# Optimization experiments

Measured on AMD Instinct MI355X. Metric: run time of the kernel, lower is better.

The kernel has to match this reference:

```python
import jax, jax.numpy as jnp
import numpy as np

NODES = 23   # 22 players + ball per frame-graph
K = 8        # random neighbors per node
B, T = 64, 128
G = B * T            # total graphs (frames)
N = G * NODES        # total nodes
D_IN, H, RH = 16, 128, 128


def setup_inputs() -> dict:
    key = jax.random.key(0)
    ks = jax.random.split(key, 10)
    x = jax.random.normal(ks[0], (N, D_IN), jnp.float32)
    # per-graph random edges: dst = each node repeated K times, src = random node in same graph
    src_local = jax.random.randint(ks[1], (G, NODES * K), 0, NODES)
    dst_local = jnp.tile(jnp.repeat(jnp.arange(NODES), K)[None, :], (G, 1))
    off = (jnp.arange(G) * NODES)[:, None]
    edge_index = jnp.stack([(src_local + off).reshape(-1),
                            (dst_local + off).reshape(-1)]).astype(jnp.int32)
    runner_idx = jax.random.randint(ks[2], (G,), 0, NODES, dtype=jnp.int32)
    sc = lambda k, sh: (jax.random.normal(k, sh, jnp.float32) * 0.05)
    return {
        'x': x, 'edge_index': edge_index, 'runner_idx': runner_idx,
        'W1': sc(ks[3], (D_IN, H)), 'b1': jnp.zeros((H,), jnp.float32),
        'W2': sc(ks[4], (H, H)),    'b2': jnp.zeros((H,), jnp.float32),
        'W_ih': sc(ks[5], (3 * RH, H)), 'W_hh': sc(ks[6], (3 * RH, RH)),
        'b_ih': jnp.zeros((3 * RH,), jnp.float32), 'b_hh': jnp.zeros((3 * RH,), jnp.float32),
        'Wp': sc(ks[7], (RH, 2)), 'bp': jnp.zeros((2,), jnp.float32),
    }


def _gcn_conv(h, edge_index, W, b):
    # PyG GCNConv: add self-loops, symmetric normalization, scatter-sum
    h = h @ W
    loop = jnp.arange(N, dtype=edge_index.dtype)
    s = jnp.concatenate([edge_index[0], loop])
    d = jnp.concatenate([edge_index[1], loop])
    deg = jax.ops.segment_sum(jnp.ones_like(s, h.dtype), d, num_segments=N)
    dinv = jnp.where(deg > 0, jax.lax.rsqrt(deg), 0.0)
    norm = dinv[s] * dinv[d]                      # [E+N]
    out = jax.ops.segment_sum(h[s] * norm[:, None], d, num_segments=N)
    return out + b


def _gru(seq, W_ih, W_hh, b_ih, b_hh):
    # torch GRU: gates in r,z,n order
    xg = seq @ W_ih.T + b_ih                      # [B,T,3RH]
    def step(hprev, xt):
        gh = hprev @ W_hh.T + b_hh
        xr, xz, xn = jnp.split(xt, 3, axis=-1)
        hr, hz, hn = jnp.split(gh, 3, axis=-1)
        r = jax.nn.sigmoid(xr + hr)
        z = jax.nn.sigmoid(xz + hz)
        n = jnp.tanh(xn + r * hn)
        hnew = (1.0 - z) * n + z * hprev
        return hnew, hnew
    h0 = jnp.zeros((seq.shape[0], RH), seq.dtype)
    _, outs = jax.lax.scan(step, h0, jnp.swapaxes(xg, 0, 1))
    return jnp.swapaxes(outs, 0, 1)               # [B,T,RH]


def reference(x, edge_index, runner_idx, W1, b1, W2, b2,
              W_ih, W_hh, b_ih, b_hh, Wp, bp):
    h = jax.nn.relu(_gcn_conv(x, edge_index, W1, b1))
    h = jax.nn.relu(_gcn_conv(h, edge_index, W2, b2))
    # fused equivalent of the per-graph nonzero()/indexing loop:
    runner_global = jnp.arange(G, dtype=jnp.int32) * NODES + runner_idx
    seq = h[runner_global].reshape(B, T, H)       # all lengths == T, padding is a no-op
    out = _gru(seq, W_ih, W_hh, b_ih, b_hh)
    return out @ Wp + bp                          # [B,T,2]
```

## Files before the change

### kernel.cpp

```cpp
#include <hip/hip_runtime.h>
#include <hip/hip_bf16.h>
#include <math.h>

#define GG 8192
#define NODESN 23
#define KK 8
#define DIN 16
#define HH 128
#define RHH 128
#define EPG (NODESN*KK)
#define TTT 128
#define BBB 64

__global__ __launch_bounds__(256) void gcn_fused(
    const float* __restrict__ x, const int* __restrict__ esrc,
    const int* __restrict__ runner,
    const float* __restrict__ W1, const float* __restrict__ b1,
    const float* __restrict__ W2, const float* __restrict__ b2,
    float* __restrict__ seq)
{
    __shared__ float xs[NODESN * DIN];
    __shared__ float W1s[DIN * HH];
    __shared__ int   srcs[EPG];
    __shared__ float t1[NODESN * HH];
    __shared__ float b1s[HH];
    __shared__ float hsum[HH];
    __shared__ float red[256];

    const int g = blockIdx.x;
    const int tid = threadIdx.x;

    for (int i = tid; i < NODESN * DIN; i += 256) xs[i] = x[g * NODESN * DIN + i];
    for (int i = tid; i < DIN * HH; i += 256)     W1s[i] = W1[i];
    for (int i = tid; i < EPG; i += 256)          srcs[i] = esrc[g * EPG + i] - g * NODESN;
    if (tid < HH) b1s[tid] = b1[tid];
    __syncthreads();

    for (int idx = tid; idx < NODESN * HH; idx += 256) {
        int n = idx >> 7, j = idx & 127;
        float acc = 0.f;
        #pragma unroll
        for (int k = 0; k < DIN; k += 4) {
            float4 xv = *(const float4*)&xs[n * DIN + k];
            acc = fmaf(xv.x, W1s[(k+0)*HH + j],
                  fmaf(xv.y, W1s[(k+1)*HH + j],
                  fmaf(xv.z, W1s[(k+2)*HH + j],
                  fmaf(xv.w, W1s[(k+3)*HH + j], acc))));
        }
        t1[idx] = acc;
    }
    __syncthreads();

    const int r = runner[g];
    {
        const int j = tid & 127, sgrp = tid >> 7;
        float part = 0.f;
        for (int slot = sgrp; slot < 9; slot += 2) {
            int node = (slot < 8) ? srcs[r * KK + slot] : r;
            float acc = t1[node * HH + j];
            #pragma unroll
            for (int k = 0; k < KK; k++) acc += t1[srcs[node * KK + k] * HH + j];
            part += fmaxf(acc * (1.f / 9.f) + b1s[j], 0.f);
        }
        red[tid] = part;
    }
    __syncthreads();
    if (tid < HH) hsum[tid] = red[tid] + red[tid + 128];
    __syncthreads();

    {
        const int j = tid & 127, kh = tid >> 7;
        float acc = 0.f;
        #pragma unroll
        for (int kq = 0; kq < 16; kq++) {
            int k = kh * 64 + kq * 4;
            float4 hv = *(const float4*)&hsum[k];
            acc = fmaf(hv.x, W2[(k+0)*HH + j],
                  fmaf(hv.y, W2[(k+1)*HH + j],
                  fmaf(hv.z, W2[(k+2)*HH + j],
                  fmaf(hv.w, W2[(k+3)*HH + j], acc))));
        }
        red[tid] = acc;
    }
    __syncthreads();
    if (tid < HH)
        seq[(size_t)g * HH + tid] =
            fmaxf((red[tid] + red[tid + 128]) * (1.f / 9.f) + b2[tid], 0.f);
}

__global__ void transpose_wih(const float* __restrict__ W, float* __restrict__ WT)
{
    int idx = blockIdx.x * 256 + threadIdx.x;
    if (idx < 3 * RHH * RHH) {
        int jj = idx / RHH, kk = idx - jj * RHH;
        WT[kk * (3 * RHH) + jj] = W[idx];
    }
}

__global__ __launch_bounds__(384) void xg_kernel(
    const float* __restrict__ seq, const float* __restrict__ WT,
    const float* __restrict__ b_ih, float* __restrict__ xg)
{
    const int tid = threadIdx.x;
    const int m0 = blockIdx.x * 8;
    const float* srow = seq + (size_t)m0 * RHH;
    float acc[8];
    const float bv = b_ih[tid];
    #pragma unroll
    for (int mi = 0; mi < 8; mi++) acc[mi] = bv;
    for (int k = 0; k < RHH; k += 4) {
        float w0 = WT[(k+0)*384 + tid];
        float w1 = WT[(k+1)*384 + tid];
        float w2 = WT[(k+2)*384 + tid];
        float w3 = WT[(k+3)*384 + tid];
        #pragma unroll
        for (int mi = 0; mi < 8; mi++) {
            float4 sv = *(const float4*)(srow + mi * RHH + k);
            acc[mi] = fmaf(sv.x, w0, fmaf(sv.y, w1, fmaf(sv.z, w2, fmaf(sv.w, w3, acc[mi]))));
        }
    }
    #pragma unroll
    for (int mi = 0; mi < 8; mi++)
        xg[(size_t)(m0 + mi) * 384 + tid] = acc[mi];
}

__global__ __launch_bounds__(768) void gru_kernel(
    const float* __restrict__ xg, const float* __restrict__ W_hh,
    const float* __restrict__ b_hh, const float* __restrict__ Wp,
    const float* __restrict__ bp, float* __restrict__ out)
{
    __shared__ float h_hist[(TTT + 1) * RHH];
    __shared__ float gh_s[3 * RHH];
    __shared__ float part_s[3 * RHH];

    const int b = blockIdx.x;
    const int tid = threadIdx.x;
    const int half = tid / 384;
    const int j = tid - half * 384;

    float w[64];
    const float* wrow = W_hh + (size_t)j * RHH + half * 64;
    #pragma unroll
    for (int q = 0; q < 16; q++) {
        float4 wv = *(const float4*)(wrow + 4 * q);
        w[4*q+0] = wv.x; w[4*q+1] = wv.y; w[4*q+2] = wv.z; w[4*q+3] = wv.w;
    }
    const float bhh = b_hh[j];

    if (tid < RHH) h_hist[tid] = 0.f;
    __syncthreads();

    const float* xrow = xg + (size_t)b * TTT * 3 * RHH;

    for (int t = 0; t < TTT; t++) {
        const float* hs = &h_hist[t * RHH + half * 64];
        float acc = 0.f;
        #pragma unroll
        for (int q = 0; q < 16; q++) {
            float4 hv = *(const float4*)(hs + 4 * q);
            acc = fmaf(hv.x, w[4*q+0],
                  fmaf(hv.y, w[4*q+1],
                  fmaf(hv.z, w[4*q+2],
                  fmaf(hv.w, w[4*q+3], acc))));
        }
        if (half) part_s[j] = acc;
        __syncthreads();
        if (!half) gh_s[j] = acc + part_s[j] + bhh;
        __syncthreads();

        if (tid < RHH) {
            const int i = tid;
            float xr = xrow[t * 384 + i];
            float xz = xrow[t * 384 + RHH + i];
            float xn = xrow[t * 384 + 2 * RHH + i];
            float hr = gh_s[i], hz = gh_s[RHH + i], hn = gh_s[2 * RHH + i];
            float rg = 1.f / (1.f + expf(-(xr + hr)));
            float zg = 1.f / (1.f + expf(-(xz + hz)));
            float ng = tanhf(fmaf(rg, hn, xn));
            float hnew = fmaf(zg, h_hist[t * RHH + i], (1.f - zg) * ng);
            h_hist[(t + 1) * RHH + i] = hnew;
        }
        __syncthreads();
    }

    for (int idx = tid; idx < TTT * 2; idx += 768) {
        int t = idx >> 1, c = idx & 1;
        float acc = bp[c];
        for (int i = 0; i < RHH; i++)
            acc = fmaf(h_hist[(t + 1) * RHH + i], Wp[i * 2 + c], acc);
        out[((size_t)b * TTT + t) * 2 + c] = acc;
    }
}

extern "C" void kernel_launch(void* const* d_in, const int* in_sizes, int n_in,
                              void* d_out, int out_size, void* d_ws, size_t ws_size,
                              hipStream_t stream)
{
    const float* x      = (const float*)d_in[0];
    const int*   eidx   = (const int*)d_in[1];
    const int*   runner = (const int*)d_in[2];
    const float* W1     = (const float*)d_in[3];
    const float* b1     = (const float*)d_in[4];
    const float* W2     = (const float*)d_in[5];
    const float* b2     = (const float*)d_in[6];
    const float* W_ih   = (const float*)d_in[7];
    const float* W_hh   = (const float*)d_in[8];
    const float* b_ih   = (const float*)d_in[9];
    const float* b_hh   = (const float*)d_in[10];
    const float* Wp     = (const float*)d_in[11];
    const float* bp     = (const float*)d_in[12];
    float* out = (float*)d_out;

    float* seq = (float*)d_ws;
    float* xg  = seq + (size_t)GG * HH;
    float* WT  = xg + (size_t)GG * 3 * RHH;

    transpose_wih<<<192, 256, 0, stream>>>(W_ih, WT);
    gcn_fused<<<GG, 256, 0, stream>>>(x, eidx, runner, W1, b1, W2, b2, seq);
    xg_kernel<<<GG / 8, 384, 0, stream>>>(seq, WT, b_ih, xg);
    gru_kernel<<<BBB, 768, 0, stream>>>(xg, W_hh, b_hh, Wp, bp, out);
}
```

Measured before the change: 295.9 us.

## Restructure GRU recurrence to one barrier per step with shuffle reductions

The GRU kernel moves to 512 threads. Each group of 4 lanes owns one hidden unit and holds all three gate rows of W_hh in registers, so the per-step split-K sum is a pair of wavefront shuffles instead of a shared-memory partial array. This cuts the loop from three barriers per timestep to one. The xg inputs are prefetched two steps ahead into a double-buffered shared array, tanh and sigmoid use fast __expf with clamping, and the h history rows are padded. The fast exp approximation adds small numerical differences, and 96 weight registers per thread raise register pressure.

```diff
diff --git a/kernel.cpp b/kernel.cpp
--- a/kernel.cpp
+++ b/kernel.cpp
@@ -11,6 +11,7 @@
 #define EPG (NODESN*KK)
 #define TTT 128
 #define BBB 64
+#define HPAD 132
 
 __global__ __launch_bounds__(256) void gcn_fused(
     const float* __restrict__ x, const int* __restrict__ esrc,
@@ -124,70 +125,93 @@
         xg[(size_t)(m0 + mi) * 384 + tid] = acc[mi];
 }
 
-__global__ __launch_bounds__(768) void gru_kernel(
+__global__ __launch_bounds__(512) void gru_kernel(
     const float* __restrict__ xg, const float* __restrict__ W_hh,
     const float* __restrict__ b_hh, const float* __restrict__ Wp,
     const float* __restrict__ bp, float* __restrict__ out)
 {
-    __shared__ float h_hist[(TTT + 1) * RHH];
-    __shared__ float gh_s[3 * RHH];
-    __shared__ float part_s[3 * RHH];
-
-    const int b = blockIdx.x;
+    __shared__ float h_hist[(TTT + 1) * HPAD];
+    __shared__ float xg_s[2][3 * RHH];
+
+    const int b   = blockIdx.x;
     const int tid = threadIdx.x;
-    const int half = tid / 384;
-    const int j = tid - half * 384;
-
-    float w[64];
-    const float* wrow = W_hh + (size_t)j * RHH + half * 64;
-    #pragma unroll
-    for (int q = 0; q < 16; q++) {
-        float4 wv = *(const float4*)(wrow + 4 * q);
-        w[4*q+0] = wv.x; w[4*q+1] = wv.y; w[4*q+2] = wv.z; w[4*q+3] = wv.w;
-    }
-    const float bhh = b_hh[j];
+    const int i   = tid >> 2;
+    const int q   = tid & 3;
+
+    float wr[32], wz[32], wn[32];
+    {
+        const float* br = W_hh + (size_t)i * RHH + q * 32;
+        const float* bz = br + (size_t)RHH * RHH;
+        const float* bn = bz + (size_t)RHH * RHH;
+        #pragma unroll
+        for (int m = 0; m < 8; m++) {
+            float4 v;
+            v = *(const float4*)(br + 4*m); wr[4*m]=v.x; wr[4*m+1]=v.y; wr[4*m+2]=v.z; wr[4*m+3]=v.w;
+            v = *(const float4*)(bz + 4*m); wz[4*m]=v.x; wz[4*m+1]=v.y; wz[4*m+2]=v.z; wz[4*m+3]=v.w;
+            v = *(const float4*)(bn + 4*m); wn[4*m]=v.x; wn[4*m+1]=v.y; wn[4*m+2]=v.z; wn[4*m+3]=v.w;
+        }
+    }
+    float bhr = 0.f, bhz = 0.f, bhn = 0.f;
+    if (q == 0) { bhr = b_hh[i]; bhz = b_hh[RHH + i]; bhn = b_hh[2 * RHH + i]; }
 
     if (tid < RHH) h_hist[tid] = 0.f;
-    __syncthreads();
-
-    const float* xrow = xg + (size_t)b * TTT * 3 * RHH;
+    const float* xbase = xg + (size_t)b * TTT * 3 * RHH;
+    float xnext = 0.f;
+    if (tid < 3 * RHH) {
+        xg_s[0][tid] = xbase[tid];
+        xnext = xbase[3 * RHH + tid];
+    }
+    float hprev = 0.f;
+    __syncthreads();
 
     for (int t = 0; t < TTT; t++) {
-        const float* hs = &h_hist[t * RHH + half * 64];
-        float acc = 0.f;
-        #pragma unroll
-        for (int q = 0; q < 16; q++) {
-            float4 hv = *(const float4*)(hs + 4 * q);
-            acc = fmaf(hv.x, w[4*q+0],
-                  fmaf(hv.y, w[4*q+1],
-                  fmaf(hv.z, w[4*q+2],
-                  fmaf(hv.w, w[4*q+3], acc))));
-        }
-        if (half) part_s[j] = acc;
+        const float* hs = &h_hist[t * HPAD + q * 32];
+        float ar = 0.f, az = 0.f, an = 0.f;
+        #pragma unroll
+        for (int m = 0; m < 8; m++) {
+            float4 hv = *(const float4*)(hs + 4 * m);
+            ar = fmaf(hv.x, wr[4*m], fmaf(hv.y, wr[4*m+1], fmaf(hv.z, wr[4*m+2], fmaf(hv.w, wr[4*m+3], ar))));
+            az = fmaf(hv.x, wz[4*m], fmaf(hv.y, wz[4*m+1], fmaf(hv.z, wz[4*m+2], fmaf(hv.w, wz[4*m+3], az))));
+            an = fmaf(hv.x, wn[4*m], fmaf(hv.y, wn[4*m+1], fmaf(hv.z, wn[4*m+2], fmaf(hv.w, wn[4*m+3], an))));
+        }
+
+        if (tid < 3 * RHH) {
+            xg_s[(t + 1) & 1][tid] = xnext;
+            xnext = (t + 2 < TTT) ? xbase[(size_t)(t + 2) * 3 * RHH + tid] : 0.f;
+        }
+
+        ar += __shfl_xor(ar, 1); ar += __shfl_xor(ar, 2);
+        az += __shfl_xor(az, 1); az += __shfl_xor(az, 2);
+        an += __shfl_xor(an, 1); an += __shfl_xor(an, 2);
+
+        if (q == 0) {
+            const float* xr_s = xg_s[t & 1];
+            float xr = xr_s[i], xz = xr_s[RHH + i], xn = xr_s[2 * RHH + i];
+            float sr = xr + ar + bhr;
+            float sz = xz + az + bhz;
+            float rg = 1.f / (1.f + __expf(-sr));
+            float zg = 1.f / (1.f + __expf(-sz));
+            float tv = fmaf(rg, an + bhn, xn);
+            tv = fminf(fmaxf(tv, -15.f), 15.f);
+            float e2 = __expf(-2.f * tv);
+            float ng = (1.f - e2) / (1.f + e2);
+            hprev = fmaf(zg, hprev, (1.f - zg) * ng);
+            h_hist[(t + 1) * HPAD + i] = hprev;
+        }
         __syncthreads();
-        if (!half) gh_s[j] = acc + part_s[j] + bhh;
-        __syncthreads();
-
-        if (tid < RHH) {
-            const int i = tid;
-            float xr = xrow[t * 384 + i];
-            float xz = xrow[t * 384 + RHH + i];
-            float xn = xrow[t * 384 + 2 * RHH + i];
-            float hr = gh_s[i], hz = gh_s[RHH + i], hn = gh_s[2 * RHH + i];
-            float rg = 1.f / (1.f + expf(-(xr + hr)));
-            float zg = 1.f / (1.f + expf(-(xz + hz)));
-            float ng = tanhf(fmaf(rg, hn, xn));
-            float hnew = fmaf(zg, h_hist[t * RHH + i], (1.f - zg) * ng);
-            h_hist[(t + 1) * RHH + i] = hnew;
-        }
-        __syncthreads();
-    }
-
-    for (int idx = tid; idx < TTT * 2; idx += 768) {
+    }
+
+    if (tid < 2 * RHH) xg_s[0][tid] = Wp[tid];
+    if (tid < 2)       xg_s[1][tid] = bp[tid];
+    __syncthreads();
+
+    for (int idx = tid; idx < TTT * 2; idx += 512) {
         int t = idx >> 1, c = idx & 1;
-        float acc = bp[c];
-        for (int i = 0; i < RHH; i++)
-            acc = fmaf(h_hist[(t + 1) * RHH + i], Wp[i * 2 + c], acc);
+        float acc = xg_s[1][c];
+        const float* hrow = &h_hist[(t + 1) * HPAD];
+        #pragma unroll 4
+        for (int ii = 0; ii < RHH; ii++)
+            acc = fmaf(hrow[ii], xg_s[0][ii * 2 + c], acc);
         out[((size_t)b * TTT + t) * 2 + c] = acc;
     }
 }
@@ -218,5 +242,5 @@
     transpose_wih<<<192, 256, 0, stream>>>(W_ih, WT);
     gcn_fused<<<GG, 256, 0, stream>>>(x, eidx, runner, W1, b1, W2, b2, seq);
     xg_kernel<<<GG / 8, 384, 0, stream>>>(seq, WT, b_ih, xg);
-    gru_kernel<<<BBB, 768, 0, stream>>>(xg, W_hh, b_hh, Wp, bp, out);
-}
+    gru_kernel<<<BBB, 512, 0, stream>>>(xg, W_hh, b_hh, Wp, bp, out);
+}
```

New measurement: 264.9 us. -10.5%, faster.
